# Kernel optimization log

Measured on AMD Instinct MI355X. Metric: run time of the kernel, lower is better.

Reference implementation:

```python
import jax, jax.numpy as jnp
import numpy as np

EPS = 1e-10

def _iou(a, b):
    """IoU for boxes in (cx, cy, w, h) format; a, b: (..., 4)."""
    a_min = a[..., :2] - a[..., 2:] * 0.5
    a_max = a[..., :2] + a[..., 2:] * 0.5
    b_min = b[..., :2] - b[..., 2:] * 0.5
    b_max = b[..., :2] + b[..., 2:] * 0.5
    inter_wh = jnp.clip(jnp.minimum(a_max, b_max) - jnp.maximum(a_min, b_min), 0.0)
    inter = inter_wh[..., 0] * inter_wh[..., 1]
    area_a = a[..., 2] * a[..., 3]
    area_b = b[..., 2] * b[..., 3]
    return inter / (area_a + area_b - inter + EPS)

def setup_inputs() -> dict:
    key = jax.random.key(0)
    k1, k2, k3 = jax.random.split(key, 3)
    BATCH, S, C = 16384, 7, 30
    # uniform in (0.01, 1) so sqrt() of w,h channels is finite/differentiable
    preds = jax.random.uniform(k1, (BATCH, S, S, C), jnp.float32, 0.01, 1.0)
    labels = jax.random.uniform(k2, (BATCH, S, S, C), jnp.float32, 0.01, 1.0)
    obj = jax.random.bernoulli(k3, 0.15, (BATCH, S, S)).astype(jnp.float32)
    labels = labels.at[..., 4].set(obj)  # code branches on labels[...,4] == 1
    return {"preds": preds, "labels": labels}

def reference(preds, labels):
    batch = preds.shape[0]
    obj = labels[..., 4] == 1.0  # (B, S, S)
    # faithful quirk: label bbox x-coord is read transposed (labels[i, y, x, 0])
    lb0 = jnp.swapaxes(labels[..., 0], 1, 2)
    lbox = jnp.stack([lb0, labels[..., 1], labels[..., 2], labels[..., 3]], axis=-1)
    iou1 = _iou(preds[..., 0:4], lbox)
    iou2 = _iou(preds[..., 5:9], lbox)
    choose1 = iou1 > iou2
    # branch where box 1 is responsible
    b1 = (5.0 * jnp.sum((preds[..., 0:2] - labels[..., 0:2]) ** 2, -1)
          + jnp.sum((jnp.sqrt(preds[..., 2:4]) - jnp.sqrt(labels[..., 2:4])) ** 2, -1)
          + (iou1 - preds[..., 4]) ** 2
          + 0.5 * preds[..., 9] ** 2)
    # branch where box 2 is responsible (targets read from labels[...,5:9] as in source)
    b2 = (5.0 * jnp.sum((preds[..., 5:7] - labels[..., 5:7]) ** 2, -1)
          + jnp.sum((jnp.sqrt(preds[..., 7:9]) - jnp.sqrt(labels[..., 7:9])) ** 2, -1)
          + (iou2 - preds[..., 9]) ** 2
          + 0.5 * preds[..., 4] ** 2)
    cls = jnp.sum((labels[..., 10:] - preds[..., 10:]) ** 2, -1)
    obj_loss = jnp.where(choose1, b1, b2) + cls
    noobj_loss = 0.5 * (preds[..., 4] ** 2 + preds[..., 9] ** 2)
    total = jnp.sum(jnp.where(obj, obj_loss, noobj_loss))
    return total / batch
```

## Files before the change

### kernel.cpp

```cpp
#include <hip/hip_runtime.h>


#define BATCH 16384
#define S 7
#define C 30
#define NCELLS (BATCH * S * S)
#define BLOCK 256

__device__ __forceinline__ float sq(float v) { return v * v; }

__device__ __forceinline__ float iou_box(float acx, float acy, float aw, float ah,
                                         float bcx, float bcy, float bw, float bh) {
    float ax0 = acx - aw * 0.5f, ax1 = acx + aw * 0.5f;
    float ay0 = acy - ah * 0.5f, ay1 = acy + ah * 0.5f;
    float bx0 = bcx - bw * 0.5f, bx1 = bcx + bw * 0.5f;
    float by0 = bcy - bh * 0.5f, by1 = bcy + bh * 0.5f;
    float iw = fminf(ax1, bx1) - fmaxf(ax0, bx0);
    float ih = fminf(ay1, by1) - fmaxf(ay0, by0);
    iw = fmaxf(iw, 0.0f);
    ih = fmaxf(ih, 0.0f);
    float inter = iw * ih;
    float denom = aw * ah + bw * bh - inter + 1e-10f;
    return inter / denom;
}

__global__ __launch_bounds__(BLOCK) void yolo_loss_kernel(
        const float* __restrict__ preds,
        const float* __restrict__ labels,
        float* __restrict__ out) {
    int cell = blockIdx.x * BLOCK + threadIdx.x;
    float loss = 0.0f;
    if (cell < NCELLS) {
        const float* p = preds  + (size_t)cell * C;
        const float* l = labels + (size_t)cell * C;

        float pv[C], lv[C];
        #pragma unroll
        for (int i = 0; i < C / 2; ++i) {
            float2 tp = *reinterpret_cast<const float2*>(p + 2 * i);
            pv[2 * i] = tp.x; pv[2 * i + 1] = tp.y;
            float2 tl = *reinterpret_cast<const float2*>(l + 2 * i);
            lv[2 * i] = tl.x; lv[2 * i + 1] = tl.y;
        }

        int b   = cell / (S * S);
        int rem = cell - b * (S * S);
        int y   = rem / S;
        int x   = rem - y * S;
        float lb0 = labels[((size_t)b * (S * S) + x * S + y) * C];

        float iou1 = iou_box(pv[0], pv[1], pv[2], pv[3], lb0, lv[1], lv[2], lv[3]);
        float iou2 = iou_box(pv[5], pv[6], pv[7], pv[8], lb0, lv[1], lv[2], lv[3]);

        float b1 = 5.0f * (sq(pv[0] - lv[0]) + sq(pv[1] - lv[1]))
                 + sq(sqrtf(pv[2]) - sqrtf(lv[2])) + sq(sqrtf(pv[3]) - sqrtf(lv[3]))
                 + sq(iou1 - pv[4])
                 + 0.5f * pv[9] * pv[9];

        float b2 = 5.0f * (sq(pv[5] - lv[5]) + sq(pv[6] - lv[6]))
                 + sq(sqrtf(pv[7]) - sqrtf(lv[7])) + sq(sqrtf(pv[8]) - sqrtf(lv[8]))
                 + sq(iou2 - pv[9])
                 + 0.5f * pv[4] * pv[4];

        float cls = 0.0f;
        #pragma unroll
        for (int c = 10; c < C; ++c) cls += sq(lv[c] - pv[c]);

        float obj_loss   = ((iou1 > iou2) ? b1 : b2) + cls;
        float noobj_loss = 0.5f * (pv[4] * pv[4] + pv[9] * pv[9]);

        loss = (lv[4] == 1.0f) ? obj_loss : noobj_loss;
    }

    #pragma unroll
    for (int off = 32; off > 0; off >>= 1)
        loss += __shfl_down(loss, off, 64);

    __shared__ float wsum[BLOCK / 64];
    int lane = threadIdx.x & 63;
    int wv   = threadIdx.x >> 6;
    if (lane == 0) wsum[wv] = loss;
    __syncthreads();
    if (threadIdx.x == 0) {
        float s = wsum[0] + wsum[1] + wsum[2] + wsum[3];
        atomicAdd(out, s * (1.0f / (float)BATCH));
    }
}

extern "C" void kernel_launch(void* const* d_in, const int* in_sizes, int n_in,
                              void* d_out, int out_size, void* d_ws, size_t ws_size,
                              hipStream_t stream) {
    const float* preds  = (const float*)d_in[0];
    const float* labels = (const float*)d_in[1];
    float* out = (float*)d_out;

    hipMemsetAsync(out, 0, sizeof(float), stream);

    int grid = (NCELLS + BLOCK - 1) / BLOCK;
    yolo_loss_kernel<<<grid, BLOCK, 0, stream>>>(preds, labels, out);
}
```

Baseline: 212.6 us.

## Stage cell data through LDS with coalesced float4 loads

Each block now copies its 256 cells of preds and labels into shared memory using coalesced float4 loads, then each thread reads its cell's 30 values from LDS. Before, threads issued strided per-thread float2 loads. The transposed lb0 lookup reads from LDS when the partner cell lies in the same tile and falls back to global memory otherwise. The bounds check is dropped on the assumption that NCELLS divides evenly by 256. The cost is 60 KB of LDS per block, which limits occupancy, plus LDS bank conflicts from the stride-30 reads.

```diff
diff --git a/kernel.cpp b/kernel.cpp
--- a/kernel.cpp
+++ b/kernel.cpp
@@ -6,6 +6,8 @@
 #define C 30
 #define NCELLS (BATCH * S * S)
 #define BLOCK 256
+#define NC 256
+#define F4_PER_ARR (NC * C / 4)
 
 __device__ __forceinline__ float sq(float v) { return v * v; }
 
@@ -15,10 +17,8 @@
     float ay0 = acy - ah * 0.5f, ay1 = acy + ah * 0.5f;
     float bx0 = bcx - bw * 0.5f, bx1 = bcx + bw * 0.5f;
     float by0 = bcy - bh * 0.5f, by1 = bcy + bh * 0.5f;
-    float iw = fminf(ax1, bx1) - fmaxf(ax0, bx0);
-    float ih = fminf(ay1, by1) - fmaxf(ay0, by0);
-    iw = fmaxf(iw, 0.0f);
-    ih = fmaxf(ih, 0.0f);
+    float iw = fmaxf(fminf(ax1, bx1) - fmaxf(ax0, bx0), 0.0f);
+    float ih = fmaxf(fminf(ay1, by1) - fmaxf(ay0, by0), 0.0f);
     float inter = iw * ih;
     float denom = aw * ah + bw * bh - inter + 1e-10f;
     return inter / denom;
@@ -28,60 +28,81 @@
         const float* __restrict__ preds,
         const float* __restrict__ labels,
         float* __restrict__ out) {
-    int cell = blockIdx.x * BLOCK + threadIdx.x;
-    float loss = 0.0f;
-    if (cell < NCELLS) {
-        const float* p = preds  + (size_t)cell * C;
-        const float* l = labels + (size_t)cell * C;
+    __shared__ float sp[NC * C];
+    __shared__ float sl[NC * C];
 
-        float pv[C], lv[C];
-        #pragma unroll
-        for (int i = 0; i < C / 2; ++i) {
-            float2 tp = *reinterpret_cast<const float2*>(p + 2 * i);
-            pv[2 * i] = tp.x; pv[2 * i + 1] = tp.y;
-            float2 tl = *reinterpret_cast<const float2*>(l + 2 * i);
-            lv[2 * i] = tl.x; lv[2 * i + 1] = tl.y;
+    const int tid = threadIdx.x;
+    const int base_cell = blockIdx.x * NC;
+
+    const float4* gp = reinterpret_cast<const float4*>(preds  + (size_t)base_cell * C);
+    const float4* gl = reinterpret_cast<const float4*>(labels + (size_t)base_cell * C);
+    float4* s4p = reinterpret_cast<float4*>(sp);
+    float4* s4l = reinterpret_cast<float4*>(sl);
+    #pragma unroll
+    for (int k = 0; k < 8; ++k) {
+        int idx = k * BLOCK + tid;
+        if (idx < F4_PER_ARR) {
+            s4p[idx] = gp[idx];
+            s4l[idx] = gl[idx];
         }
+    }
+    __syncthreads();
 
-        int b   = cell / (S * S);
-        int rem = cell - b * (S * S);
-        int y   = rem / S;
-        int x   = rem - y * S;
-        float lb0 = labels[((size_t)b * (S * S) + x * S + y) * C];
+    const float* p = sp + tid * C;
+    const float* l = sl + tid * C;
+    float pv[C], lv[C];
+    #pragma unroll
+    for (int i = 0; i < C / 2; ++i) {
+        float2 tp = *reinterpret_cast<const float2*>(p + 2 * i);
+        pv[2 * i] = tp.x; pv[2 * i + 1] = tp.y;
+        float2 tl = *reinterpret_cast<const float2*>(l + 2 * i);
+        lv[2 * i] = tl.x; lv[2 * i + 1] = tl.y;
+    }
 
-        float iou1 = iou_box(pv[0], pv[1], pv[2], pv[3], lb0, lv[1], lv[2], lv[3]);
-        float iou2 = iou_box(pv[5], pv[6], pv[7], pv[8], lb0, lv[1], lv[2], lv[3]);
+    int cell = base_cell + tid;
+    int b    = cell / (S * S);
+    int rem  = cell - b * (S * S);
+    int y    = rem / S;
+    int x    = rem - y * S;
+    int pc   = b * (S * S) + x * S + y;
+    float lb0;
+    if (pc >= base_cell && pc < base_cell + NC) {
+        lb0 = sl[(pc - base_cell) * C];
+    } else {
+        lb0 = labels[(size_t)pc * C];
+    }
 
-        float b1 = 5.0f * (sq(pv[0] - lv[0]) + sq(pv[1] - lv[1]))
-                 + sq(sqrtf(pv[2]) - sqrtf(lv[2])) + sq(sqrtf(pv[3]) - sqrtf(lv[3]))
-                 + sq(iou1 - pv[4])
-                 + 0.5f * pv[9] * pv[9];
+    float iou1 = iou_box(pv[0], pv[1], pv[2], pv[3], lb0, lv[1], lv[2], lv[3]);
+    float iou2 = iou_box(pv[5], pv[6], pv[7], pv[8], lb0, lv[1], lv[2], lv[3]);
 
-        float b2 = 5.0f * (sq(pv[5] - lv[5]) + sq(pv[6] - lv[6]))
-                 + sq(sqrtf(pv[7]) - sqrtf(lv[7])) + sq(sqrtf(pv[8]) - sqrtf(lv[8]))
-                 + sq(iou2 - pv[9])
-                 + 0.5f * pv[4] * pv[4];
+    float b1 = 5.0f * (sq(pv[0] - lv[0]) + sq(pv[1] - lv[1]))
+             + sq(sqrtf(pv[2]) - sqrtf(lv[2])) + sq(sqrtf(pv[3]) - sqrtf(lv[3]))
+             + sq(iou1 - pv[4])
+             + 0.5f * pv[9] * pv[9];
 
-        float cls = 0.0f;
-        #pragma unroll
-        for (int c = 10; c < C; ++c) cls += sq(lv[c] - pv[c]);
+    float b2 = 5.0f * (sq(pv[5] - lv[5]) + sq(pv[6] - lv[6]))
+             + sq(sqrtf(pv[7]) - sqrtf(lv[7])) + sq(sqrtf(pv[8]) - sqrtf(lv[8]))
+             + sq(iou2 - pv[9])
+             + 0.5f * pv[4] * pv[4];
 
-        float obj_loss   = ((iou1 > iou2) ? b1 : b2) + cls;
-        float noobj_loss = 0.5f * (pv[4] * pv[4] + pv[9] * pv[9]);
+    float cls = 0.0f;
+    #pragma unroll
+    for (int c = 10; c < C; ++c) cls += sq(lv[c] - pv[c]);
 
-        loss = (lv[4] == 1.0f) ? obj_loss : noobj_loss;
-    }
+    float obj_loss   = ((iou1 > iou2) ? b1 : b2) + cls;
+    float noobj_loss = 0.5f * (pv[4] * pv[4] + pv[9] * pv[9]);
+    float loss = (lv[4] == 1.0f) ? obj_loss : noobj_loss;
 
     #pragma unroll
     for (int off = 32; off > 0; off >>= 1)
         loss += __shfl_down(loss, off, 64);
 
     __shared__ float wsum[BLOCK / 64];
-    int lane = threadIdx.x & 63;
-    int wv   = threadIdx.x >> 6;
+    int lane = tid & 63;
+    int wv   = tid >> 6;
     if (lane == 0) wsum[wv] = loss;
     __syncthreads();
-    if (threadIdx.x == 0) {
+    if (tid == 0) {
         float s = wsum[0] + wsum[1] + wsum[2] + wsum[3];
         atomicAdd(out, s * (1.0f / (float)BATCH));
     }
@@ -96,6 +117,6 @@
 
     hipMemsetAsync(out, 0, sizeof(float), stream);
 
-    int grid = (NCELLS + BLOCK - 1) / BLOCK;
+    int grid = NCELLS / NC;
     yolo_loss_kernel<<<grid, BLOCK, 0, stream>>>(preds, labels, out);
 }
```

Measured after the change: 211.1 us. Within noise of the previous version (-0.7%).
